# Performance work log

Measured on AMD Instinct MI355X. Metric: run time of the kernel, lower is better.

## Reference

```python
import jax, jax.numpy as jnp
import numpy as np

N, E, D, H1, H2 = 50000, 800000, 128, 128, 128


def setup_inputs() -> dict:
    key = jax.random.key(0)
    ks = jax.random.split(key, 9)
    s = 0.05
    return {
        "x": jax.random.normal(ks[0], (N, D), dtype=jnp.float32),
        "edge_index": jax.random.randint(ks[1], (2, E), 0, N, dtype=jnp.int64),
        "W_l1": jax.random.normal(ks[2], (D, H1), dtype=jnp.float32) * s,
        "b_l1": jnp.zeros((H1,), dtype=jnp.float32),
        "W_r1": jax.random.normal(ks[3], (D, H1), dtype=jnp.float32) * s,
        "W_l2": jax.random.normal(ks[4], (H1, H2), dtype=jnp.float32) * s,
        "b_l2": jnp.zeros((H2,), dtype=jnp.float32),
        "W_r2": jax.random.normal(ks[5], (H1, H2), dtype=jnp.float32) * s,
        "W_e": jax.random.normal(ks[6], (2 * H2, 1), dtype=jnp.float32) * s,
        "b_e": jnp.zeros((1,), dtype=jnp.float32),
    }


def _sage_conv(h, src, tgt, n_nodes, W_l, b_l, W_r):
    # PyG SAGEConv (mean aggr): out = lin_l(mean_{j in N(i)} h_j) + lin_r(h_i)
    msg = h[src]                                              # [E, F] gather
    agg = jax.ops.segment_sum(msg, tgt, num_segments=n_nodes)  # [N, F]
    cnt = jax.ops.segment_sum(jnp.ones((src.shape[0], 1), h.dtype), tgt,
                              num_segments=n_nodes)            # [N, 1]
    mean = agg / jnp.maximum(cnt, 1.0)                         # empty nbrs -> 0
    return mean @ W_l + b_l + h @ W_r


def reference(x, edge_index, W_l1, b_l1, W_r1, W_l2, b_l2, W_r2, W_e, b_e):
    src, tgt = edge_index[0], edge_index[1]
    n_nodes = x.shape[0]
    h = jax.nn.relu(_sage_conv(x, src, tgt, n_nodes, W_l1, b_l1, W_r1))
    # dropout is identity in eval mode
    h = _sage_conv(h, src, tgt, n_nodes, W_l2, b_l2, W_r2)
    z = jnp.concatenate([h[src], h[tgt]], axis=-1)  # [E, 2*H2]
    y = z @ W_e + b_e                                # [E, 1]
    return jax.nn.sigmoid(y)
```

## Files before the change

kernel.cpp:

```cpp
#include <hip/hip_runtime.h>

#define NN 50000
#define NE 800000
#define DD 128
#define BUCKETS 196
#define PB 4096
#define PBLK 196
#define EMAX 6144
#define BPAD 264
#define PACKB 6250

typedef unsigned int uint_t;
typedef unsigned short ush_t;
typedef __attribute__((ext_vector_type(8))) short short8;
typedef __attribute__((ext_vector_type(4))) float f32x4;

__device__ __forceinline__ float bflo(uint_t u) { return __uint_as_float(u << 16); }
__device__ __forceinline__ float bfhi(uint_t u) { return __uint_as_float(u & 0xffff0000u); }
__device__ __forceinline__ ush_t f2bf(float f) {
  uint_t u = __float_as_uint(f);
  u += 0x7fffu + ((u >> 16) & 1u);
  return (ush_t)(u >> 16);
}
__device__ __forceinline__ uint2 pack4(float a, float b, float c, float d) {
  uint2 o;
  o.x = (uint_t)f2bf(a) | ((uint_t)f2bf(b) << 16);
  o.y = (uint_t)f2bf(c) | ((uint_t)f2bf(d) << 16);
  return o;
}

__device__ __forceinline__ int ld_idx(const void* ei, int is64, long long i) {
  return is64 ? (int)((const long long*)ei)[i] : ((const int*)ei)[i];
}

__device__ __forceinline__ int block_incl_scan(int v, int tid, int* wsum) {
  int lane = tid & 63, wave = tid >> 6;
  int s = v;
#pragma unroll
  for (int off = 1; off < 64; off <<= 1) {
    int u = __shfl_up(s, off, 64);
    if (lane >= off) s += u;
  }
  if (lane == 63) wsum[wave] = s;
  __syncthreads();
  int base = 0;
  if (wave > 0) base += wsum[0];
  if (wave > 1) base += wsum[1];
  if (wave > 2) base += wsum[2];
  return base + s;
}

__global__ __launch_bounds__(256) void prep_k(
    const float* __restrict__ x, ush_t* __restrict__ xb,
    const float* __restrict__ Wl1, const float* __restrict__ Wr1,
    const float* __restrict__ Wl2, const float* __restrict__ Wr2,
    ush_t* __restrict__ Wt1, ush_t* __restrict__ Wt2,
    const void* __restrict__ ei, int* __restrict__ flag,
    int* __restrict__ bcur) {
  int tid = threadIdx.x;
  int blk = blockIdx.x;
  if (blk < PACKB) {
    int i = blk * 256 + tid;
    float4 v = reinterpret_cast<const float4*>(x)[i];
    reinterpret_cast<uint2*>(xb)[i] = pack4(v.x, v.y, v.z, v.w);
    return;
  }
  blk -= PACKB;
  if (blk < 256) {
    int e = blk * 256 + tid;
    int layer = e >> 15;
    int r = e & 32767;
    int col = r >> 8;
    int k = r & 255;
    const float* Wl = layer ? Wl2 : Wl1;
    const float* Wr = layer ? Wr2 : Wr1;
    float v = (k < DD) ? Wl[k * DD + col] : Wr[(k - DD) * DD + col];
    ush_t* Wt = layer ? Wt2 : Wt1;
    Wt[col * 256 + k] = f2bf(v);
    return;
  }
  bcur[tid] = 0;
  if (tid == 0) {
    const unsigned long long* p = (const unsigned long long*)ei;
    int is64 = 1;
    for (int i = 0; i < 64; ++i)
      if (p[i] >= (1ull << 32)) { is64 = 0; break; }
    *flag = is64;
  }
}

__global__ __launch_bounds__(256) void part_k(const void* __restrict__ ei,
                                              const int* __restrict__ flag,
                                              int* __restrict__ bcur,
                                              uint_t* __restrict__ pbuf) {
  __shared__ int hist[256];
  __shared__ int basel[256];
  __shared__ int cur[256];
  __shared__ int gbase[256];
  __shared__ int wsum[4];
  __shared__ uint_t buf[PB];
  __shared__ unsigned char bbuf[PB];
  int tid = threadIdx.x;
  hist[tid] = 0;
  __syncthreads();
  int is64 = *flag;
  long long base = (long long)blockIdx.x * PB;
  uint_t pv[PB / 256];
#pragma unroll
  for (int i = 0; i < PB / 256; ++i) {
    long long e = base + i * 256 + tid;
    if (e < NE) {
      int s = ld_idx(ei, is64, e);
      int d = ld_idx(ei, is64, (long long)NE + e);
      pv[i] = ((uint_t)(d >> 8) << 24) | ((uint_t)(d & 255) << 16) | (uint_t)s;
      atomicAdd(&hist[d >> 8], 1);
    } else {
      pv[i] = 0xFFFFFFFFu;
    }
  }
  __syncthreads();
  int hv = hist[tid];
  int incl = block_incl_scan(hv, tid, wsum);
  basel[tid] = incl - hv;
  cur[tid] = incl - hv;
  if (hv > 0) gbase[tid] = atomicAdd(&bcur[tid], hv);
  __syncthreads();
#pragma unroll
  for (int i = 0; i < PB / 256; ++i) {
    uint_t p = pv[i];
    if (p != 0xFFFFFFFFu) {
      int b = p >> 24;
      int r = atomicAdd(&cur[b], 1);
      buf[r] = p & 0xFFFFFFu;
      bbuf[r] = (unsigned char)b;
    }
  }
  __syncthreads();
  int total = basel[255] + hist[255];
  for (int j = tid; j < total; j += 256) {
    int b = bbuf[j];
    int slot = gbase[b] + (j - basel[b]);
    if (slot < EMAX) pbuf[(size_t)b * EMAX + slot] = buf[j];
  }
}

__global__ __launch_bounds__(256) void csr_k(const uint_t* __restrict__ pbuf,
                                             const int* __restrict__ bcur,
                                             int* __restrict__ offsets,
                                             int* __restrict__ srclist) {
  __shared__ int cnt[256];
  __shared__ int scur[256];
  __shared__ int wsum[4];
  __shared__ int sgb, scnt, stot;
  __shared__ uint_t ebuf[EMAX];
  int tid = threadIdx.x;
  int b = blockIdx.x;
  int v = 0;
  if (tid < BUCKETS) {
    v = bcur[tid];
    if (v > EMAX) v = EMAX;
  }
  int incl = block_incl_scan(v, tid, wsum);
  if (tid == b) { sgb = incl - v; scnt = v; }
  if (tid == BUCKETS - 1) stot = incl;
  cnt[tid] = 0;
  __syncthreads();
  int gb = sgb;
  int ecnt = scnt;
  for (int j = tid; j < ecnt; j += 256) {
    uint_t e = pbuf[(size_t)b * EMAX + j];
    ebuf[j] = e;
    atomicAdd(&cnt[(e >> 16) & 255], 1);
  }
  __syncthreads();
  int c = cnt[tid];
  int incl2 = block_incl_scan(c, tid, wsum);
  int ex = incl2 - c;
  scur[tid] = ex;
  int node = b * 256 + tid;
  if (node < NN) offsets[node] = gb + ex;
  if (b == BUCKETS - 1 && tid == 0) offsets[NN] = stot;
  __syncthreads();
  for (int j = tid; j < ecnt; j += 256) {
    uint_t e = ebuf[j];
    int p = atomicAdd(&scur[(e >> 16) & 255], 1);
    srclist[gb + p] = (int)(e & 0xFFFFu);
  }
}

__global__ __launch_bounds__(256) void agg_k(const ush_t* __restrict__ featb,
                                             const int* __restrict__ srclist,
                                             const int* __restrict__ offsets,
                                             ush_t* __restrict__ meanb) {
  int t = blockIdx.x * 256 + threadIdx.x;
  int node = t >> 5;
  int lane = t & 31;
  int f = lane << 2;
  int beg = offsets[node];
  int end = offsets[node + 1];
  float4 acc = make_float4(0.f, 0.f, 0.f, 0.f);
  for (int c = beg; c < end; c += 32) {
    int idx = c + lane;
    int sl = (idx < end) ? srclist[idx] : 0;
    int m = min(32, end - c);
    int jj = 0;
    for (; jj + 4 <= m; jj += 4) {
      int s0 = __shfl(sl, jj, 32);
      int s1 = __shfl(sl, jj + 1, 32);
      int s2 = __shfl(sl, jj + 2, 32);
      int s3 = __shfl(sl, jj + 3, 32);
      uint2 v0 = *reinterpret_cast<const uint2*>(featb + (size_t)s0 * DD + f);
      uint2 v1 = *reinterpret_cast<const uint2*>(featb + (size_t)s1 * DD + f);
      uint2 v2 = *reinterpret_cast<const uint2*>(featb + (size_t)s2 * DD + f);
      uint2 v3 = *reinterpret_cast<const uint2*>(featb + (size_t)s3 * DD + f);
      acc.x += bflo(v0.x); acc.y += bfhi(v0.x); acc.z += bflo(v0.y); acc.w += bfhi(v0.y);
      acc.x += bflo(v1.x); acc.y += bfhi(v1.x); acc.z += bflo(v1.y); acc.w += bfhi(v1.y);
      acc.x += bflo(v2.x); acc.y += bfhi(v2.x); acc.z += bflo(v2.y); acc.w += bfhi(v2.y);
      acc.x += bflo(v3.x); acc.y += bfhi(v3.x); acc.z += bflo(v3.y); acc.w += bfhi(v3.y);
    }
    for (; jj < m; ++jj) {
      int s = __shfl(sl, jj, 32);
      uint2 v = *reinterpret_cast<const uint2*>(featb + (size_t)s * DD + f);
      acc.x += bflo(v.x); acc.y += bfhi(v.x);
      acc.z += bflo(v.y); acc.w += bfhi(v.y);
    }
  }
  float inv = 1.0f / fmaxf((float)(end - beg), 1.0f);
  *reinterpret_cast<uint2*>(meanb + (size_t)node * DD + f) =
      pack4(acc.x * inv, acc.y * inv, acc.z * inv, acc.w * inv);
}

#define MFMA_CORE(A0PTR, A1PTR, WTPTR)                                         \
  int tid = threadIdx.x;                                                       \
  int lane = tid & 63;                                                         \
  int wave = tid >> 6;                                                         \
  int n15 = lane & 15, quad = lane >> 4;                                       \
  int nb = blockIdx.x * 64;                                                    \
  for (int it = 0; it < 16; ++it) {                                            \
    int i = it * 256 + tid;                                                    \
    int col = i >> 5, c = i & 31;                                              \
    *reinterpret_cast<short8*>(&sB[col * BPAD + c * 8]) =                      \
        reinterpret_cast<const short8*>(WTPTR)[i];                             \
  }                                                                            \
  __syncthreads();                                                             \
  int row = nb + wave * 16 + n15;                                              \
  int arow = (row < NN) ? row : (NN - 1);                                      \
  const ush_t* a0 = A0PTR + (size_t)arow * DD;                                 \
  const ush_t* a1 = A1PTR + (size_t)arow * DD;                                 \
  f32x4 acc[8];                                                                \
  _Pragma("unroll")                                                            \
  for (int t = 0; t < 8; ++t) acc[t] = (f32x4){0.f, 0.f, 0.f, 0.f};           \
  _Pragma("unroll")                                                            \
  for (int c = 0; c < 8; ++c) {                                                \
    const ush_t* ap = (c < 4) ? (a0 + c * 32 + quad * 8)                       \
                              : (a1 + (c - 4) * 32 + quad * 8);                \
    short8 af = *reinterpret_cast<const short8*>(ap);                          \
    int kb = c * 32 + quad * 8;                                                \
    _Pragma("unroll")                                                          \
    for (int t = 0; t < 8; ++t) {                                              \
      short8 bf = *reinterpret_cast<const short8*>(&sB[(t * 16 + n15) * BPAD + kb]); \
      acc[t] = __builtin_amdgcn_mfma_f32_16x16x32_bf16(af, bf, acc[t], 0, 0, 0); \
    }                                                                          \
  }

__global__ __launch_bounds__(256, 2) void sage_l1(
    const ush_t* __restrict__ meanb, const ush_t* __restrict__ xb,
    const ush_t* __restrict__ Wt1, const float* __restrict__ bl,
    ush_t* __restrict__ h1b) {
  __shared__ ush_t sB[128 * BPAD];
  MFMA_CORE(meanb, xb, Wt1)
#pragma unroll
  for (int t = 0; t < 8; ++t) {
    int col = t * 16 + n15;
    float b = bl[col];
#pragma unroll
    for (int reg = 0; reg < 4; ++reg) {
      int r = nb + wave * 16 + quad * 4 + reg;
      if (r < NN)
        h1b[(size_t)r * DD + col] = f2bf(fmaxf(acc[t][reg] + b, 0.f));
    }
  }
}

__global__ __launch_bounds__(256, 2) void sage_l2(
    const ush_t* __restrict__ meanb, const ush_t* __restrict__ h1b,
    const ush_t* __restrict__ Wt2, const float* __restrict__ bl,
    const float* __restrict__ We, float* __restrict__ s1,
    float* __restrict__ s2) {
  __shared__ ush_t sB[128 * BPAD];
  MFMA_CORE(meanb, h1b, Wt2)
  float p1[4] = {0.f, 0.f, 0.f, 0.f};
  float p2[4] = {0.f, 0.f, 0.f, 0.f};
#pragma unroll
  for (int t = 0; t < 8; ++t) {
    int col = t * 16 + n15;
    float b = bl[col];
    float w1 = We[col];
    float w2 = We[DD + col];
#pragma unroll
    for (int reg = 0; reg < 4; ++reg) {
      float v = acc[t][reg] + b;
      p1[reg] += v * w1;
      p2[reg] += v * w2;
    }
  }
#pragma unroll
  for (int reg = 0; reg < 4; ++reg) {
    float v1 = p1[reg], v2 = p2[reg];
    for (int off = 8; off > 0; off >>= 1) {
      v1 += __shfl_down(v1, off, 16);
      v2 += __shfl_down(v2, off, 16);
    }
    int r = nb + wave * 16 + quad * 4 + reg;
    if (n15 == 0 && r < NN) {
      s1[r] = v1;
      s2[r] = v2;
    }
  }
}

__global__ __launch_bounds__(256) void edge_k(const void* __restrict__ ei,
                                              const int* __restrict__ flag,
                                              const float* __restrict__ s1,
                                              const float* __restrict__ s2,
                                              const float* __restrict__ be,
                                              float* __restrict__ out) {
  int e = blockIdx.x * 256 + threadIdx.x;
  int is64 = *flag;
  int s = ld_idx(ei, is64, e);
  int d = ld_idx(ei, is64, (long long)NE + e);
  float v = s1[s] + s2[d] + be[0];
  out[e] = 1.0f / (1.0f + __expf(-v));
}

extern "C" void kernel_launch(void* const* d_in, const int* in_sizes, int n_in,
                              void* d_out, int out_size, void* d_ws, size_t ws_size,
                              hipStream_t stream) {
  const float* x   = (const float*)d_in[0];
  const void*  ei  = d_in[1];
  const float* Wl1 = (const float*)d_in[2];
  const float* bl1 = (const float*)d_in[3];
  const float* Wr1 = (const float*)d_in[4];
  const float* Wl2 = (const float*)d_in[5];
  const float* bl2 = (const float*)d_in[6];
  const float* Wr2 = (const float*)d_in[7];
  const float* We  = (const float*)d_in[8];
  const float* be  = (const float*)d_in[9];
  float* out = (float*)d_out;

  int* bcur    = (int*)d_ws;
  int* flag    = bcur + 256;
  int* offsets = flag + 4;
  uint_t* pbuf = (uint_t*)(offsets + NN + 4);
  int* srclist = (int*)(pbuf + (size_t)BUCKETS * EMAX);
  ush_t* xb    = (ush_t*)(srclist + NE);
  ush_t* meanb = xb + (size_t)NN * DD;
  ush_t* h1b   = meanb + (size_t)NN * DD;
  float* s1    = (float*)(h1b + (size_t)NN * DD);
  float* s2    = s1 + NN;
  ush_t* Wt1   = (ush_t*)(s2 + NN);
  ush_t* Wt2   = Wt1 + 32768;

  prep_k<<<PACKB + 257, 256, 0, stream>>>(x, xb, Wl1, Wr1, Wl2, Wr2, Wt1, Wt2,
                                          ei, flag, bcur);
  part_k<<<PBLK, 256, 0, stream>>>(ei, flag, bcur, pbuf);
  csr_k<<<BUCKETS, 256, 0, stream>>>(pbuf, bcur, offsets, srclist);

  int gemm_blocks = (NN + 63) / 64;
  agg_k<<<(NN * 32) / 256, 256, 0, stream>>>(xb, srclist, offsets, meanb);
  sage_l1<<<gemm_blocks, 256, 0, stream>>>(meanb, xb, Wt1, bl1, h1b);

  agg_k<<<(NN * 32) / 256, 256, 0, stream>>>(h1b, srclist, offsets, meanb);
  sage_l2<<<gemm_blocks, 256, 0, stream>>>(meanb, h1b, Wt2, bl2, We, s1, s2);

  edge_k<<<NE / 256, 256, 0, stream>>>(ei, flag, s1, s2, be, out);
}
```

Before: 221.8 us.

## Fuse prep with partition, widen aggregation loads, pack edge indices for scoring

Merges the prep and partition kernels into one launch. The index-width flag is now detected per wave with a ballot, and the bucket counters are cleared with a memset. The partition pass also writes a packed 32-bit (dst<<16|src) edge array, which the final edge kernel reads in place of the int64 edge_index. s1/s2 are stored interleaved as float2. Aggregation now uses 16 lanes per node with 16-byte loads instead of 32 lanes with 8-byte loads, so each gathered row needs fewer, wider loads, at the cost of more registers per lane and less parallelism per node.

```diff
diff --git a/kernel.cpp b/kernel.cpp
--- a/kernel.cpp
+++ b/kernel.cpp
@@ -22,15 +22,18 @@
   u += 0x7fffu + ((u >> 16) & 1u);
   return (ush_t)(u >> 16);
 }
-__device__ __forceinline__ uint2 pack4(float a, float b, float c, float d) {
-  uint2 o;
-  o.x = (uint_t)f2bf(a) | ((uint_t)f2bf(b) << 16);
-  o.y = (uint_t)f2bf(c) | ((uint_t)f2bf(d) << 16);
-  return o;
+__device__ __forceinline__ uint_t pack2(float a, float b) {
+  return (uint_t)f2bf(a) | ((uint_t)f2bf(b) << 16);
 }
 
 __device__ __forceinline__ int ld_idx(const void* ei, int is64, long long i) {
   return is64 ? (int)((const long long*)ei)[i] : ((const int*)ei)[i];
+}
+
+__device__ __forceinline__ int detect64(const void* ei) {
+  const unsigned long long* p = (const unsigned long long*)ei;
+  unsigned long long w = p[threadIdx.x & 63];
+  return __ballot((w >> 32) != 0) == 0ull ? 1 : 0;
 }
 
 __device__ __forceinline__ int block_incl_scan(int v, int tid, int* wsum) {
@@ -50,23 +53,34 @@
   return base + s;
 }
 
-__global__ __launch_bounds__(256) void prep_k(
+__global__ __launch_bounds__(256) void prep_part_k(
+    const void* __restrict__ ei, int* __restrict__ bcur,
+    uint_t* __restrict__ pbuf, uint_t* __restrict__ epk,
     const float* __restrict__ x, ush_t* __restrict__ xb,
     const float* __restrict__ Wl1, const float* __restrict__ Wr1,
     const float* __restrict__ Wl2, const float* __restrict__ Wr2,
-    ush_t* __restrict__ Wt1, ush_t* __restrict__ Wt2,
-    const void* __restrict__ ei, int* __restrict__ flag,
-    int* __restrict__ bcur) {
+    ush_t* __restrict__ Wt1, ush_t* __restrict__ Wt2) {
+  __shared__ int hist[256];
+  __shared__ int basel[256];
+  __shared__ int cur[256];
+  __shared__ int gbase[256];
+  __shared__ int wsum[4];
+  __shared__ uint_t buf[PB];
+  __shared__ unsigned char bbuf[PB];
   int tid = threadIdx.x;
   int blk = blockIdx.x;
-  if (blk < PACKB) {
-    int i = blk * 256 + tid;
-    float4 v = reinterpret_cast<const float4*>(x)[i];
-    reinterpret_cast<uint2*>(xb)[i] = pack4(v.x, v.y, v.z, v.w);
-    return;
-  }
-  blk -= PACKB;
-  if (blk < 256) {
+  if (blk >= PBLK) {
+    blk -= PBLK;
+    if (blk < PACKB) {
+      int i = blk * 256 + tid;
+      float4 v = reinterpret_cast<const float4*>(x)[i];
+      uint2 o;
+      o.x = pack2(v.x, v.y);
+      o.y = pack2(v.z, v.w);
+      reinterpret_cast<uint2*>(xb)[i] = o;
+      return;
+    }
+    blk -= PACKB;
     int e = blk * 256 + tid;
     int layer = e >> 15;
     int r = e & 32767;
@@ -79,32 +93,10 @@
     Wt[col * 256 + k] = f2bf(v);
     return;
   }
-  bcur[tid] = 0;
-  if (tid == 0) {
-    const unsigned long long* p = (const unsigned long long*)ei;
-    int is64 = 1;
-    for (int i = 0; i < 64; ++i)
-      if (p[i] >= (1ull << 32)) { is64 = 0; break; }
-    *flag = is64;
-  }
-}
-
-__global__ __launch_bounds__(256) void part_k(const void* __restrict__ ei,
-                                              const int* __restrict__ flag,
-                                              int* __restrict__ bcur,
-                                              uint_t* __restrict__ pbuf) {
-  __shared__ int hist[256];
-  __shared__ int basel[256];
-  __shared__ int cur[256];
-  __shared__ int gbase[256];
-  __shared__ int wsum[4];
-  __shared__ uint_t buf[PB];
-  __shared__ unsigned char bbuf[PB];
-  int tid = threadIdx.x;
+  int is64 = detect64(ei);
   hist[tid] = 0;
   __syncthreads();
-  int is64 = *flag;
-  long long base = (long long)blockIdx.x * PB;
+  long long base = (long long)blk * PB;
   uint_t pv[PB / 256];
 #pragma unroll
   for (int i = 0; i < PB / 256; ++i) {
@@ -113,6 +105,7 @@
       int s = ld_idx(ei, is64, e);
       int d = ld_idx(ei, is64, (long long)NE + e);
       pv[i] = ((uint_t)(d >> 8) << 24) | ((uint_t)(d & 255) << 16) | (uint_t)s;
+      epk[e] = ((uint_t)d << 16) | (uint_t)s;
       atomicAdd(&hist[d >> 8], 1);
     } else {
       pv[i] = 0xFFFFFFFFu;
@@ -193,41 +186,49 @@
                                              const int* __restrict__ offsets,
                                              ush_t* __restrict__ meanb) {
   int t = blockIdx.x * 256 + threadIdx.x;
-  int node = t >> 5;
-  int lane = t & 31;
-  int f = lane << 2;
+  int node = t >> 4;
+  int lane = t & 15;
+  int f = lane << 3;
   int beg = offsets[node];
   int end = offsets[node + 1];
-  float4 acc = make_float4(0.f, 0.f, 0.f, 0.f);
-  for (int c = beg; c < end; c += 32) {
+  float a0 = 0.f, a1 = 0.f, a2 = 0.f, a3 = 0.f, a4 = 0.f, a5 = 0.f, a6 = 0.f, a7 = 0.f;
+  for (int c = beg; c < end; c += 16) {
     int idx = c + lane;
     int sl = (idx < end) ? srclist[idx] : 0;
-    int m = min(32, end - c);
+    int m = min(16, end - c);
     int jj = 0;
     for (; jj + 4 <= m; jj += 4) {
-      int s0 = __shfl(sl, jj, 32);
-      int s1 = __shfl(sl, jj + 1, 32);
-      int s2 = __shfl(sl, jj + 2, 32);
-      int s3 = __shfl(sl, jj + 3, 32);
-      uint2 v0 = *reinterpret_cast<const uint2*>(featb + (size_t)s0 * DD + f);
-      uint2 v1 = *reinterpret_cast<const uint2*>(featb + (size_t)s1 * DD + f);
-      uint2 v2 = *reinterpret_cast<const uint2*>(featb + (size_t)s2 * DD + f);
-      uint2 v3 = *reinterpret_cast<const uint2*>(featb + (size_t)s3 * DD + f);
-      acc.x += bflo(v0.x); acc.y += bfhi(v0.x); acc.z += bflo(v0.y); acc.w += bfhi(v0.y);
-      acc.x += bflo(v1.x); acc.y += bfhi(v1.x); acc.z += bflo(v1.y); acc.w += bfhi(v1.y);
-      acc.x += bflo(v2.x); acc.y += bfhi(v2.x); acc.z += bflo(v2.y); acc.w += bfhi(v2.y);
-      acc.x += bflo(v3.x); acc.y += bfhi(v3.x); acc.z += bflo(v3.y); acc.w += bfhi(v3.y);
+      int s0 = __shfl(sl, jj, 16);
+      int s1 = __shfl(sl, jj + 1, 16);
+      int s2 = __shfl(sl, jj + 2, 16);
+      int s3 = __shfl(sl, jj + 3, 16);
+      uint4 v0 = *reinterpret_cast<const uint4*>(featb + (size_t)s0 * DD + f);
+      uint4 v1 = *reinterpret_cast<const uint4*>(featb + (size_t)s1 * DD + f);
+      uint4 v2 = *reinterpret_cast<const uint4*>(featb + (size_t)s2 * DD + f);
+      uint4 v3 = *reinterpret_cast<const uint4*>(featb + (size_t)s3 * DD + f);
+      a0 += bflo(v0.x); a1 += bfhi(v0.x); a2 += bflo(v0.y); a3 += bfhi(v0.y);
+      a4 += bflo(v0.z); a5 += bfhi(v0.z); a6 += bflo(v0.w); a7 += bfhi(v0.w);
+      a0 += bflo(v1.x); a1 += bfhi(v1.x); a2 += bflo(v1.y); a3 += bfhi(v1.y);
+      a4 += bflo(v1.z); a5 += bfhi(v1.z); a6 += bflo(v1.w); a7 += bfhi(v1.w);
+      a0 += bflo(v2.x); a1 += bfhi(v2.x); a2 += bflo(v2.y); a3 += bfhi(v2.y);
+      a4 += bflo(v2.z); a5 += bfhi(v2.z); a6 += bflo(v2.w); a7 += bfhi(v2.w);
+      a0 += bflo(v3.x); a1 += bfhi(v3.x); a2 += bflo(v3.y); a3 += bfhi(v3.y);
+      a4 += bflo(v3.z); a5 += bfhi(v3.z); a6 += bflo(v3.w); a7 += bfhi(v3.w);
     }
     for (; jj < m; ++jj) {
-      int s = __shfl(sl, jj, 32);
-      uint2 v = *reinterpret_cast<const uint2*>(featb + (size_t)s * DD + f);
-      acc.x += bflo(v.x); acc.y += bfhi(v.x);
-      acc.z += bflo(v.y); acc.w += bfhi(v.y);
+      int s = __shfl(sl, jj, 16);
+      uint4 v = *reinterpret_cast<const uint4*>(featb + (size_t)s * DD + f);
+      a0 += bflo(v.x); a1 += bfhi(v.x); a2 += bflo(v.y); a3 += bfhi(v.y);
+      a4 += bflo(v.z); a5 += bfhi(v.z); a6 += bflo(v.w); a7 += bfhi(v.w);
     }
   }
   float inv = 1.0f / fmaxf((float)(end - beg), 1.0f);
-  *reinterpret_cast<uint2*>(meanb + (size_t)node * DD + f) =
-      pack4(acc.x * inv, acc.y * inv, acc.z * inv, acc.w * inv);
+  uint4 o;
+  o.x = pack2(a0 * inv, a1 * inv);
+  o.y = pack2(a2 * inv, a3 * inv);
+  o.z = pack2(a4 * inv, a5 * inv);
+  o.w = pack2(a6 * inv, a7 * inv);
+  *reinterpret_cast<uint4*>(meanb + (size_t)node * DD + f) = o;
 }
 
 #define MFMA_CORE(A0PTR, A1PTR, WTPTR)                                         \
@@ -285,8 +286,7 @@
 __global__ __launch_bounds__(256, 2) void sage_l2(
     const ush_t* __restrict__ meanb, const ush_t* __restrict__ h1b,
     const ush_t* __restrict__ Wt2, const float* __restrict__ bl,
-    const float* __restrict__ We, float* __restrict__ s1,
-    float* __restrict__ s2) {
+    const float* __restrict__ We, float2* __restrict__ s12) {
   __shared__ ush_t sB[128 * BPAD];
   MFMA_CORE(meanb, h1b, Wt2)
   float p1[4] = {0.f, 0.f, 0.f, 0.f};
@@ -312,24 +312,19 @@
       v2 += __shfl_down(v2, off, 16);
     }
     int r = nb + wave * 16 + quad * 4 + reg;
-    if (n15 == 0 && r < NN) {
-      s1[r] = v1;
-      s2[r] = v2;
-    }
-  }
-}
-
-__global__ __launch_bounds__(256) void edge_k(const void* __restrict__ ei,
-                                              const int* __restrict__ flag,
-                                              const float* __restrict__ s1,
-                                              const float* __restrict__ s2,
+    if (n15 == 0 && r < NN) s12[r] = make_float2(v1, v2);
+  }
+}
+
+__global__ __launch_bounds__(256) void edge_k(const uint_t* __restrict__ epk,
+                                              const float2* __restrict__ s12,
                                               const float* __restrict__ be,
                                               float* __restrict__ out) {
   int e = blockIdx.x * 256 + threadIdx.x;
-  int is64 = *flag;
-  int s = ld_idx(ei, is64, e);
-  int d = ld_idx(ei, is64, (long long)NE + e);
-  float v = s1[s] + s2[d] + be[0];
+  uint_t p = epk[e];
+  float2 a = s12[p & 0xFFFFu];
+  float2 b = s12[p >> 16];
+  float v = a.x + b.y + be[0];
   out[e] = 1.0f / (1.0f + __expf(-v));
 }
 
@@ -349,29 +344,28 @@
   float* out = (float*)d_out;
 
   int* bcur    = (int*)d_ws;
-  int* flag    = bcur + 256;
-  int* offsets = flag + 4;
-  uint_t* pbuf = (uint_t*)(offsets + NN + 4);
+  int* offsets = bcur + 256;
+  uint_t* epk  = (uint_t*)(offsets + 50004);
+  uint_t* pbuf = epk + NE;
   int* srclist = (int*)(pbuf + (size_t)BUCKETS * EMAX);
   ush_t* xb    = (ush_t*)(srclist + NE);
   ush_t* meanb = xb + (size_t)NN * DD;
   ush_t* h1b   = meanb + (size_t)NN * DD;
-  float* s1    = (float*)(h1b + (size_t)NN * DD);
-  float* s2    = s1 + NN;
-  ush_t* Wt1   = (ush_t*)(s2 + NN);
+  float2* s12  = (float2*)(h1b + (size_t)NN * DD);
+  ush_t* Wt1   = (ush_t*)((float*)s12 + 2 * NN);
   ush_t* Wt2   = Wt1 + 32768;
 
-  prep_k<<<PACKB + 257, 256, 0, stream>>>(x, xb, Wl1, Wr1, Wl2, Wr2, Wt1, Wt2,
-                                          ei, flag, bcur);
-  part_k<<<PBLK, 256, 0, stream>>>(ei, flag, bcur, pbuf);
+  hipMemsetAsync(bcur, 0, 256 * sizeof(int), stream);
+  prep_part_k<<<PBLK + PACKB + 256, 256, 0, stream>>>(
+      ei, bcur, pbuf, epk, x, xb, Wl1, Wr1, Wl2, Wr2, Wt1, Wt2);
   csr_k<<<BUCKETS, 256, 0, stream>>>(pbuf, bcur, offsets, srclist);
 
   int gemm_blocks = (NN + 63) / 64;
-  agg_k<<<(NN * 32) / 256, 256, 0, stream>>>(xb, srclist, offsets, meanb);
+  agg_k<<<(NN * 16) / 256, 256, 0, stream>>>(xb, srclist, offsets, meanb);
   sage_l1<<<gemm_blocks, 256, 0, stream>>>(meanb, xb, Wt1, bl1, h1b);
 
-  agg_k<<<(NN * 32) / 256, 256, 0, stream>>>(h1b, srclist, offsets, meanb);
-  sage_l2<<<gemm_blocks, 256, 0, stream>>>(meanb, h1b, Wt2, bl2, We, s1, s2);
-
-  edge_k<<<NE / 256, 256, 0, stream>>>(ei, flag, s1, s2, be, out);
-}
+  agg_k<<<(NN * 16) / 256, 256, 0, stream>>>(h1b, srclist, offsets, meanb);
+  sage_l2<<<gemm_blocks, 256, 0, stream>>>(meanb, h1b, Wt2, bl2, We, s12);
+
+  edge_k<<<NE / 256, 256, 0, stream>>>(epk, s12, be, out);
+}
```

Measured after the change: 220.2 us. No clear change (-0.7%).
